# Kernel optimization log

Measured on AMD Instinct MI355X. Metric: run time of the kernel, lower is better.

Reference implementation:

```python
import jax, jax.numpy as jnp
import numpy as np

DIM = 192
HEADS = 6
HEAD_DIM = DIM // HEADS
WS = 8            # window size
N = WS * WS       # tokens per window
IN_CC = 16        # top-k kept keys per query
B, H, W = 8, 64, 64
NEG = -100.0      # value used by the torch code for masked logits
EPS_NORM = 1e-12  # F.normalize eps
EPS_LN = 1e-5     # nn.LayerNorm eps


def _rel_pos_index(ws):
    coords = np.stack(np.meshgrid(np.arange(ws), np.arange(ws), indexing='ij'))  # (2,ws,ws)
    cf = coords.reshape(2, -1)
    rel = (cf[:, :, None] - cf[:, None, :]).transpose(1, 2, 0).astype(np.int64)  # (N,N,2)
    rel[:, :, 0] += ws - 1
    rel[:, :, 1] += ws - 1
    rel[:, :, 0] *= 2 * ws - 1
    return jnp.asarray(rel.sum(-1))  # (N,N) indices into (2ws-1)^2 table

REL_IDX = _rel_pos_index(WS)


def _layer_norm(x, g, b):
    mu = jnp.mean(x, -1, keepdims=True)
    var = jnp.mean(jnp.square(x - mu), -1, keepdims=True)
    return (x - mu) * jax.lax.rsqrt(var + EPS_LN) * g + b


def _l2n(x):
    n = jnp.sqrt(jnp.sum(jnp.square(x), -1, keepdims=True))
    return x / jnp.maximum(n, EPS_NORM)


def setup_inputs() -> dict:
    key = jax.random.key(0)
    ks = jax.random.split(key, 8)
    s = 0.02
    return {
        'x': jax.random.normal(ks[0], (B, DIM, H, W), jnp.float32),
        'norm1_g': jnp.ones((DIM,), jnp.float32),
        'norm1_b': jnp.zeros((DIM,), jnp.float32),
        'qkv_w': jax.random.normal(ks[1], (3 * DIM, DIM), jnp.float32) * s,
        'qkv_b': jnp.zeros((3 * DIM,), jnp.float32),
        'proj_w': jax.random.normal(ks[2], (DIM, DIM), jnp.float32) * s,
        'proj_b': jnp.zeros((DIM,), jnp.float32),
        'rpb_table': jax.random.normal(ks[3], ((2 * WS - 1) ** 2, HEADS), jnp.float32) * s,
        'temperature': jnp.ones((HEADS, 1, 1), jnp.float32),
        'norm2_g': jnp.ones((DIM,), jnp.float32),
        'norm2_b': jnp.zeros((DIM,), jnp.float32),
        'fc1_w': jax.random.normal(ks[4], (4 * DIM, DIM), jnp.float32) * s,
        'fc1_b': jnp.zeros((4 * DIM,), jnp.float32),
        'fc2_w': jax.random.normal(ks[5], (DIM, 4 * DIM), jnp.float32) * s,
        'fc2_b': jnp.zeros((DIM,), jnp.float32),
    }


def reference(x, norm1_g, norm1_b, qkv_w, qkv_b, proj_w, proj_b, rpb_table,
              temperature, norm2_g, norm2_b, fc1_w, fc1_b, fc2_w, fc2_b):
    b, c, h, w = x.shape
    # (B,C,H,W) -> (B,L,C), pre-norm (note: the torch code norms the shortcut too)
    xs = jnp.transpose(x.reshape(b, c, h * w), (0, 2, 1))
    shortcut = _layer_norm(xs, norm1_g, norm1_b)  # (B,L,C)

    # window partition: (B,H,W,C) -> (B*nWh*nWw, N, C); shift_size=0, no padding (H,W % WS == 0)
    xin = shortcut.reshape(b, h // WS, WS, w // WS, WS, c)
    xin = jnp.transpose(xin, (0, 1, 3, 2, 4, 5)).reshape(-1, N, c)
    B_ = xin.shape[0]

    qkv = (xin @ qkv_w.T + qkv_b).reshape(B_, N, 3, HEADS, HEAD_DIM)
    qkv = jnp.transpose(qkv, (2, 0, 3, 1, 4))  # (3, B_, h, N, d)
    q, k, v = qkv[0], qkv[1], qkv[2]

    # cosine attention with learned per-head temperature
    attn = jnp.einsum('bhnd,bhmd->bhnm', _l2n(q), _l2n(k)) * temperature  # (B_,h,N,N)

    # top-k sparsification: keep IN_CC largest logits per query (threshold == kth value;
    # equivalent to the torch topk+scatter mask for distinct values)
    kth = jax.lax.top_k(attn, IN_CC)[0][..., -1:]
    attn = jnp.where(attn >= kth, attn, NEG)

    # relative position bias gather: (N,N,h) -> (h,N,N)
    rpb = jnp.transpose(rpb_table[REL_IDX], (2, 0, 1))
    attn = jax.nn.softmax(attn + rpb[None], axis=-1)

    out = jnp.einsum('bhnm,bhmd->bhnd', attn, v)
    out = jnp.transpose(out, (0, 2, 1, 3)).reshape(B_, N, c)
    out = out @ proj_w.T + proj_b

    # window reverse -> (B, L, C)
    out = out.reshape(b, h // WS, w // WS, WS, WS, c)
    out = jnp.transpose(out, (0, 1, 3, 2, 4, 5)).reshape(b, h * w, c)

    x2 = shortcut + out  # drop_path = identity (eval)
    hdn = _layer_norm(x2, norm2_g, norm2_b)
    hdn = jax.nn.gelu(hdn @ fc1_w.T + fc1_b, approximate=False) @ fc2_w.T + fc2_b
    x2 = x2 + hdn

    # back to (B,C,H,W)
    return jnp.transpose(x2, (0, 2, 1)).reshape(b, c, h, w)
```

## Files before the change

### kernel.cpp

```cpp
#include <hip/hip_runtime.h>
#include <hip/hip_bf16.h>
#include <math.h>

#define DIM     192
#define HEADS   6
#define HEAD_DIM 32
#define NTOK    64
#define IN_CC   16
#define TTOT    32768
#define NWIN    512

using bf16x8 = __attribute__((ext_vector_type(8))) short;
using f32x4  = __attribute__((ext_vector_type(4))) float;
typedef unsigned short ushort_t;

__device__ __forceinline__ ushort_t f2b(float f) {
    unsigned u = __float_as_uint(f);
    u += 0x7fffu + ((u >> 16) & 1u);
    return (ushort_t)(u >> 16);
}
__device__ __forceinline__ unsigned pk2(float a, float b) {
    return (unsigned)f2b(a) | ((unsigned)f2b(b) << 16);
}

__global__ __launch_bounds__(256) void cvt_all_kernel(
    const float* __restrict__ s0, const float* __restrict__ s1,
    const float* __restrict__ s2, const float* __restrict__ s3,
    ushort_t* __restrict__ d0, ushort_t* __restrict__ d1,
    ushort_t* __restrict__ d2, ushort_t* __restrict__ d3)
{
    const int bid = blockIdx.x;
    const float* src; ushort_t* dst; int off, K;
    if (bid < 108)      { src = s0; dst = d0; off = bid;       K = 192; }
    else if (bid < 144) { src = s1; dst = d1; off = bid - 108; K = 192; }
    else if (bid < 288) { src = s2; dst = d2; off = bid - 144; K = 192; }
    else                { src = s3; dst = d3; off = bid - 288; K = 768; }
    const int K8 = K >> 3;
    const int d  = (off * 256 + threadIdx.x) * 4;
    const int frag = d >> 7, win = d & 127;
    const int m16w = win >> 3, k7 = win & 7;
    const int oblk = frag / K8, kblk = frag - oblk * K8;
    const int o = oblk * 16 + m16w, k = kblk * 8 + k7;
    float4 v = *(const float4*)(src + (size_t)o * K + k);
    ushort4 ov;
    ov.x = f2b(v.x); ov.y = f2b(v.y); ov.z = f2b(v.z); ov.w = f2b(v.w);
    *(ushort4*)(dst + d) = ov;
}

__global__ __launch_bounds__(256) void ln1_kernel(
    const float* __restrict__ x, const float* __restrict__ g,
    const float* __restrict__ bb, float* __restrict__ outp,
    ushort_t* __restrict__ outh)
{
    __shared__ float xs[64][193];
    __shared__ float mu_s[64], rs_s[64];
    __shared__ float gs[192], bs[192];
    const int tid = threadIdx.x;
    const int t0  = blockIdx.x * 64;
    const int b   = t0 >> 12;
    const int hw0 = t0 & 4095;
    if (tid < 192) { gs[tid] = g[tid]; bs[tid] = bb[tid]; }
    const int tok = tid & 63, qq = tid >> 6;
    const float* xb = x + (size_t)b * (DIM * 4096) + hw0 + tok;
    #pragma unroll
    for (int it = 0; it < 48; ++it) {
        int c = it * 4 + qq;
        xs[tok][c] = xb[(size_t)c * 4096];
    }
    __syncthreads();
    const int tok2 = tid >> 2, p = tid & 3;
    float sum = 0.f;
    #pragma unroll
    for (int c = 0; c < 48; ++c) sum += xs[tok2][p * 48 + c];
    sum += __shfl_xor(sum, 1);
    sum += __shfl_xor(sum, 2);
    const float m = sum * (1.0f / 192.0f);
    float ss = 0.f;
    #pragma unroll
    for (int c = 0; c < 48; ++c) { float d = xs[tok2][p * 48 + c] - m; ss += d * d; }
    ss += __shfl_xor(ss, 1);
    ss += __shfl_xor(ss, 2);
    if (p == 0) {
        mu_s[tok2] = m;
        rs_s[tok2] = 1.0f / sqrtf(ss * (1.0f / 192.0f) + 1e-5f);
    }
    __syncthreads();
    float* ob = outp + (size_t)t0 * DIM;
    ushort_t* obh = outh + (size_t)t0 * DIM;
    #pragma unroll
    for (int it = 0; it < 48; ++it) {
        int idx = it * 256 + tid;
        int tk = idx / 192, c = idx % 192;
        float v = (xs[tk][c] - mu_s[tk]) * rs_s[tk] * gs[c] + bs[c];
        ob[idx] = v;
        obh[idx] = f2b(v);
    }
}

__global__ __launch_bounds__(256) void gemm_mfma(
    const ushort_t* __restrict__ A, const ushort_t* __restrict__ Wf,
    const float* __restrict__ bias, const float* __restrict__ res,
    float* __restrict__ outf, ushort_t* __restrict__ outh,
    int N, int K, int epi)
{
    __shared__ __align__(16) float Ct[4][32][68];
    const int tid  = threadIdx.x;
    const int wave = tid >> 6, lane = tid & 63;
    const int m16 = lane & 15, quad = lane >> 4;
    const int t0 = (blockIdx.x * 4 + wave) * 64, o0 = blockIdx.y * 64;
    const int K8 = K >> 3;
    float (*Cw)[68] = Ct[wave];

    f32x4 acc[4][4];
    #pragma unroll
    for (int i = 0; i < 4; ++i)
        #pragma unroll
        for (int j = 0; j < 4; ++j)
            acc[i][j] = (f32x4)(0.0f);

    const ushort_t* Ab = A + (size_t)t0 * K + quad * 8;
    const ushort_t* Wb = Wf + (size_t)(o0 >> 4) * K8 * 128 + m16 * 8;
    for (int ks = 0; ks < K; ks += 32) {
        bf16x8 af[4], wv[4];
        #pragma unroll
        for (int i = 0; i < 4; ++i)
            af[i] = *(const bf16x8*)(Ab + (size_t)(16 * i + m16) * K + ks);
        #pragma unroll
        for (int j = 0; j < 4; ++j)
            wv[j] = *(const bf16x8*)(Wb + (size_t)(j * K8 + (ks >> 3) + quad) * 128);
        #pragma unroll
        for (int i = 0; i < 4; ++i)
            #pragma unroll
            for (int j = 0; j < 4; ++j)
                acc[i][j] = __builtin_amdgcn_mfma_f32_16x16x32_bf16(wv[j], af[i], acc[i][j], 0, 0, 0);
    }

    float4 bj[4];
    #pragma unroll
    for (int j = 0; j < 4; ++j)
        bj[j] = *(const float4*)&bias[o0 + 16 * j + quad * 4];

    #pragma unroll
    for (int p = 0; p < 2; ++p) {
        #pragma unroll
        for (int ih = 0; ih < 2; ++ih) {
            const int i = 2 * p + ih;
            #pragma unroll
            for (int j = 0; j < 4; ++j) {
                f32x4 v = acc[i][j];
                v[0] += bj[j].x; v[1] += bj[j].y; v[2] += bj[j].z; v[3] += bj[j].w;
                *(f32x4*)&Cw[ih * 16 + m16][16 * j + quad * 4] = v;
            }
        }
        if (epi == 3) {
            #pragma unroll
            for (int q = 0; q < 4; ++q) {
                const int idx = q * 64 + lane;
                const int row = idx >> 3, c8 = (idx & 7) * 8;
                float4 f0 = *(const float4*)&Cw[row][c8];
                float4 f1 = *(const float4*)&Cw[row][c8 + 4];
                uint4 w;
                w.x = pk2(f0.x, f0.y); w.y = pk2(f0.z, f0.w);
                w.z = pk2(f1.x, f1.y); w.w = pk2(f1.z, f1.w);
                *(uint4*)&outh[(size_t)(t0 + p * 32 + row) * N + o0 + c8] = w;
            }
        } else {
            #pragma unroll
            for (int q = 0; q < 8; ++q) {
                const int idx = q * 64 + lane;
                const int row = idx >> 4, c4 = (idx & 15) * 4;
                float4 vv = *(const float4*)&Cw[row][c4];
                const size_t gidx = (size_t)(t0 + p * 32 + row) * N + o0 + c4;
                if (epi == 1) {
                    const float4 rv = *(const float4*)&res[gidx];
                    vv.x += rv.x; vv.y += rv.y; vv.z += rv.z; vv.w += rv.w;
                }
                *(float4*)&outf[gidx] = vv;
            }
        }
    }
}

__global__ __launch_bounds__(256) void mlp_fused(
    const float* __restrict__ x2, const ushort_t* __restrict__ w1f,
    const ushort_t* __restrict__ w2f, const float* __restrict__ fc1_b,
    const float* __restrict__ fc2_b, const float* __restrict__ g2,
    const float* __restrict__ b2, float* __restrict__ outp)
{
    __shared__ __align__(16) char smem[43008];
    ushort_t (*h_h)[200] = (ushort_t(*)[200])smem;
    ushort_t (*a1c)[136] = (ushort_t(*)[136])(smem + 25600);
    float* gs  = (float*)(smem + 25600);
    float* bs  = gs + 192;

    const int tid  = threadIdx.x;
    const int wave = tid >> 6, lane = tid & 63;
    const int m16 = lane & 15, quad = lane >> 4;
    const int t0 = blockIdx.x * 64;
    const int b   = t0 >> 12;
    const int hw0 = t0 & 4095;

    if (tid < 192) { gs[tid] = g2[tid]; bs[tid] = b2[tid]; }
    __syncthreads();
    {
        const int tok = tid >> 2, p = tid & 3;
        const float* rp = x2 + (size_t)(t0 + tok) * DIM + p * 48;
        float xv[48];
        #pragma unroll
        for (int c4 = 0; c4 < 12; ++c4)
            *(float4*)&xv[c4 * 4] = *(const float4*)(rp + c4 * 4);
        float sum = 0.f;
        #pragma unroll
        for (int c = 0; c < 48; ++c) sum += xv[c];
        sum += __shfl_xor(sum, 1);
        sum += __shfl_xor(sum, 2);
        const float m = sum * (1.0f / 192.0f);
        float ss = 0.f;
        #pragma unroll
        for (int c = 0; c < 48; ++c) { float d = xv[c] - m; ss += d * d; }
        ss += __shfl_xor(ss, 1);
        ss += __shfl_xor(ss, 2);
        const float rs = 1.0f / sqrtf(ss * (1.0f / 192.0f) + 1e-5f);
        ushort_t* hp = &h_h[tok][p * 48];
        #pragma unroll
        for (int c2 = 0; c2 < 24; ++c2) {
            float v0 = (xv[2*c2]   - m) * rs * gs[p * 48 + 2*c2]   + bs[p * 48 + 2*c2];
            float v1 = (xv[2*c2+1] - m) * rs * gs[p * 48 + 2*c2+1] + bs[p * 48 + 2*c2+1];
            *(unsigned*)(hp + 2 * c2) = pk2(v0, v1);
        }
    }
    __syncthreads();

    f32x4 acc2[4][3];
    #pragma unroll
    for (int i = 0; i < 4; ++i)
        #pragma unroll
        for (int j = 0; j < 3; ++j)
            acc2[i][j] = (f32x4)(0.0f);

    for (int c = 0; c < 6; ++c) {
        f32x4 acc1[4][2];
        #pragma unroll
        for (int i = 0; i < 4; ++i)
            #pragma unroll
            for (int j = 0; j < 2; ++j)
                acc1[i][j] = (f32x4)(0.0f);
        const ushort_t* Wb1 = w1f + (size_t)(c * 8 + wave * 2) * 24 * 128 + m16 * 8;
        for (int ks = 0; ks < 192; ks += 32) {
            bf16x8 af[4], wv[2];
            #pragma unroll
            for (int i = 0; i < 4; ++i)
                af[i] = *(const bf16x8*)&h_h[16 * i + m16][quad * 8 + ks];
            #pragma unroll
            for (int j = 0; j < 2; ++j)
                wv[j] = *(const bf16x8*)(Wb1 + (size_t)(j * 24 + (ks >> 3) + quad) * 128);
            #pragma unroll
            for (int i = 0; i < 4; ++i)
                #pragma unroll
                for (int j = 0; j < 2; ++j)
                    acc1[i][j] = __builtin_amdgcn_mfma_f32_16x16x32_bf16(wv[j], af[i], acc1[i][j], 0, 0, 0);
        }
        float2 b1j[2];
        #pragma unroll
        for (int j = 0; j < 2; ++j) {
            const int o = c * 128 + wave * 32 + 16 * j + quad * 4;
            b1j[j] = make_float2(0.f, 0.f);
        }
        #pragma unroll
        for (int j = 0; j < 2; ++j) {
            const int o = c * 128 + wave * 32 + 16 * j + quad * 4;
            const float4 bv = *(const float4*)&fc1_b[o];
            #pragma unroll
            for (int i = 0; i < 4; ++i) {
                f32x4 v = acc1[i][j];
                v[0] += bv.x; v[1] += bv.y; v[2] += bv.z; v[3] += bv.w;
                #pragma unroll
                for (int r = 0; r < 4; ++r) {
                    float xg = v[r];
                    float e1 = __expf(xg * (1.5957691f + 0.0713548f * xg * xg)) + 1.0f;
                    v[r] = xg - xg * __builtin_amdgcn_rcpf(e1);
                }
                uint2 pkd;
                pkd.x = pk2(v[0], v[1]); pkd.y = pk2(v[2], v[3]);
                *(uint2*)&a1c[16 * i + m16][wave * 32 + 16 * j + quad * 4] = pkd;
            }
        }
        __syncthreads();
        const ushort_t* Wb2 = w2f + (size_t)(wave * 3) * 96 * 128 + m16 * 8;
        for (int ks = 0; ks < 128; ks += 32) {
            bf16x8 af2[4], wv2[3];
            #pragma unroll
            for (int i = 0; i < 4; ++i)
                af2[i] = *(const bf16x8*)&a1c[16 * i + m16][quad * 8 + ks];
            #pragma unroll
            for (int j = 0; j < 3; ++j)
                wv2[j] = *(const bf16x8*)(Wb2 + (size_t)(j * 96 + c * 16 + (ks >> 3) + quad) * 128);
            #pragma unroll
            for (int i = 0; i < 4; ++i)
                #pragma unroll
                for (int j = 0; j < 3; ++j)
                    acc2[i][j] = __builtin_amdgcn_mfma_f32_16x16x32_bf16(wv2[j], af2[i], acc2[i][j], 0, 0, 0);
        }
        __syncthreads();
    }

    float (*Cw)[68] = (float(*)[68])(smem + wave * 8704);
    float4 b2j[3];
    #pragma unroll
    for (int j = 0; j < 3; ++j)
        b2j[j] = *(const float4*)&fc2_b[wave * 48 + 16 * j + quad * 4];
    #pragma unroll
    for (int p = 0; p < 2; ++p) {
        #pragma unroll
        for (int ih = 0; ih < 2; ++ih) {
            const int i = 2 * p + ih;
            #pragma unroll
            for (int j = 0; j < 3; ++j) {
                f32x4 v = acc2[i][j];
                v[0] += b2j[j].x; v[1] += b2j[j].y; v[2] += b2j[j].z; v[3] += b2j[j].w;
                *(f32x4*)&Cw[ih * 16 + m16][16 * j + quad * 4] = v;
            }
        }
        #pragma unroll
        for (int q = 0; q < 6; ++q) {
            const int idx = q * 64 + lane;
            const int cc = idx >> 3, t4 = (idx & 7) * 4;
            const int o  = wave * 48 + cc;
            const int tb = t0 + p * 32 + t4;
            float4 vv;
            vv.x = Cw[t4 + 0][cc] + x2[(size_t)(tb + 0) * DIM + o];
            vv.y = Cw[t4 + 1][cc] + x2[(size_t)(tb + 1) * DIM + o];
            vv.z = Cw[t4 + 2][cc] + x2[(size_t)(tb + 2) * DIM + o];
            vv.w = Cw[t4 + 3][cc] + x2[(size_t)(tb + 3) * DIM + o];
            *(float4*)&outp[(size_t)b * (DIM * 4096) + (size_t)o * 4096
                            + hw0 + p * 32 + t4] = vv;
        }
    }
}

__global__ __launch_bounds__(64) void attn_mfma_kernel(
    const ushort_t* __restrict__ qkvh, const float* __restrict__ rpb_table,
    const float* __restrict__ temp, ushort_t* __restrict__ outb)
{
    __shared__ __align__(16) char smem[16016];
    ushort_t* Qh  = (ushort_t*)smem;
    ushort_t* Kh  = (ushort_t*)(smem + 5120);
    float*    Ss  = (float*)smem;
    ushort_t* Pl  = (ushort_t*)smem;
    ushort_t* Vt  = (ushort_t*)(smem + 10240);
    float*    ksb = (float*)(smem + 14848);
    float*    rpb = (float*)(smem + 15104);

    const int n   = threadIdx.x;
    const int win = blockIdx.x;
    const int h   = blockIdx.y;
    const int b   = win >> 6;
    const int wh  = (win >> 3) & 7, ww = win & 7;
    const int i1  = n >> 3, j1 = n & 7;
    const int t   = b * 4096 + (wh * 8 + i1) * 64 + (ww * 8 + j1);
    const ushort_t* base = qkvh + (size_t)t * 576 + h * 32;
    const int m16 = n & 15, quad = n >> 4;

    unsigned qu[16], ku[16], vu[16];
    #pragma unroll
    for (int c = 0; c < 4; ++c) {
        ((uint4*)qu)[c] = *(const uint4*)(base + 8 * c);
        ((uint4*)ku)[c] = *(const uint4*)(base + 192 + 8 * c);
        ((uint4*)vu)[c] = *(const uint4*)(base + 384 + 8 * c);
    }
    float sq = 0.f, sk = 0.f;
    #pragma unroll
    for (int c = 0; c < 16; ++c) {
        float a0 = __uint_as_float(qu[c] << 16);
        float a1 = __uint_as_float(qu[c] & 0xffff0000u);
        sq += a0 * a0 + a1 * a1;
        float b0 = __uint_as_float(ku[c] << 16);
        float b1 = __uint_as_float(ku[c] & 0xffff0000u);
        sk += b0 * b0 + b1 * b1;
    }
    const float qs  = temp[h] / fmaxf(sqrtf(sq), 1e-12f);
    const float ksc = 1.0f / fmaxf(sqrtf(sk), 1e-12f);

    #pragma unroll
    for (int c = 0; c < 4; ++c) {
        *(uint4*)&Qh[n * 40 + 8 * c] = ((uint4*)qu)[c];
        *(uint4*)&Kh[n * 40 + 8 * c] = ((uint4*)ku)[c];
    }
    const int vslot = 4 * m16 + quad;
    #pragma unroll
    for (int d = 0; d < 16; ++d) {
        Vt[(2 * d) * 72 + vslot]     = (ushort_t)(vu[d] & 0xffffu);
        Vt[(2 * d + 1) * 72 + vslot] = (ushort_t)(vu[d] >> 16);
    }
    ksb[vslot] = ksc;
    for (int r = n; r < 225; r += 64) rpb[r] = rpb_table[r * 6 + h];
    __syncthreads();

    bf16x8 aq[4], bk[4];
    #pragma unroll
    for (int i = 0; i < 4; ++i) aq[i] = *(const bf16x8*)&Qh[(16*i + m16) * 40 + quad * 8];
    #pragma unroll
    for (int j = 0; j < 4; ++j) bk[j] = *(const bf16x8*)&Kh[(16*j + m16) * 40 + quad * 8];
    f32x4 acc[4][4];
    #pragma unroll
    for (int i = 0; i < 4; ++i)
        #pragma unroll
        for (int j = 0; j < 4; ++j)
            acc[i][j] = __builtin_amdgcn_mfma_f32_16x16x32_bf16(aq[i], bk[j], (f32x4)(0.0f), 0, 0, 0);
    __syncthreads();

    float s[64];
    #pragma unroll
    for (int i = 0; i < 2; ++i)
        #pragma unroll
        for (int r = 0; r < 4; ++r) {
            f32x4 vv = { acc[i][0][r], acc[i][1][r], acc[i][2][r], acc[i][3][r] };
            *(f32x4*)&Ss[(16 * i + 4 * quad + r) * 68 + 4 * m16] = vv;
        }
    __syncthreads();
    if (n < 32) {
        #pragma unroll
        for (int c = 0; c < 16; ++c)
            *(float4*)&s[4 * c] = *(const float4*)&Ss[n * 68 + 4 * c];
    }
    __syncthreads();
    #pragma unroll
    for (int i = 2; i < 4; ++i)
        #pragma unroll
        for (int r = 0; r < 4; ++r) {
            f32x4 vv = { acc[i][0][r], acc[i][1][r], acc[i][2][r], acc[i][3][r] };
            *(f32x4*)&Ss[(16 * (i - 2) + 4 * quad + r) * 68 + 4 * m16] = vv;
        }
    __syncthreads();
    if (n >= 32) {
        #pragma unroll
        for (int c = 0; c < 16; ++c)
            *(float4*)&s[4 * c] = *(const float4*)&Ss[(n - 32) * 68 + 4 * c];
    }

    #pragma unroll
    for (int c = 0; c < 16; ++c) {
        float4 kv = *(const float4*)&ksb[4 * c];
        s[4*c+0] *= qs * kv.x; s[4*c+1] *= qs * kv.y;
        s[4*c+2] *= qs * kv.z; s[4*c+3] *= qs * kv.w;
    }

    float thr = 1e30f;
    for (int it = 0; it < IN_CC; ++it) {
        float mx = -1e30f;
        #pragma unroll
        for (int m = 0; m < 64; ++m) {
            float vv = (s[m] < thr) ? s[m] : -1e30f;
            mx = fmaxf(mx, vv);
        }
        thr = mx;
    }

    const int basen = i1 * 15 + j1;
    float mx = -1e30f;
    #pragma unroll
    for (int c = 0; c < 64; ++c) {
        const int m = 16 * (c & 3) + (c >> 2);
        const int i2 = m >> 3, j2 = m & 7;
        float vv = ((s[c] >= thr) ? s[c] : -100.0f)
                 + rpb[basen + (7 - i2) * 15 + (7 - j2)];
        s[c] = vv;
        mx = fmaxf(mx, vv);
    }
    float sum = 0.f;
    #pragma unroll
    for (int c = 0; c < 64; ++c) { float e = __expf(s[c] - mx); s[c] = e; sum += e; }
    const float inv = 1.0f / sum;
    #pragma unroll
    for (int c = 0; c < 64; ++c) s[c] *= inv;

    __syncthreads();
    #pragma unroll
    for (int gix = 0; gix < 8; ++gix) {
        uint4 w;
        w.x = pk2(s[8*gix+0], s[8*gix+1]); w.y = pk2(s[8*gix+2], s[8*gix+3]);
        w.z = pk2(s[8*gix+4], s[8*gix+5]); w.w = pk2(s[8*gix+6], s[8*gix+7]);
        *(uint4*)&Pl[n * 72 + 8 * gix] = w;
    }
    __syncthreads();

    f32x4 o[4][2];
    #pragma unroll
    for (int i = 0; i < 4; ++i)
        #pragma unroll
        for (int j2 = 0; j2 < 2; ++j2)
            o[i][j2] = (f32x4)(0.0f);
    #pragma unroll
    for (int kh = 0; kh < 64; kh += 32) {
        bf16x8 pa[4], vb[2];
        #pragma unroll
        for (int i = 0; i < 4; ++i)
            pa[i] = *(const bf16x8*)&Pl[(16*i + m16) * 72 + kh + quad * 8];
        #pragma unroll
        for (int j2 = 0; j2 < 2; ++j2)
            vb[j2] = *(const bf16x8*)&Vt[(16*j2 + m16) * 72 + kh + quad * 8];
        #pragma unroll
        for (int i = 0; i < 4; ++i)
            #pragma unroll
            for (int j2 = 0; j2 < 2; ++j2)
                o[i][j2] = __builtin_amdgcn_mfma_f32_16x16x32_bf16(pa[i], vb[j2], o[i][j2], 0, 0, 0);
    }

    #pragma unroll
    for (int i = 0; i < 4; ++i) {
        #pragma unroll
        for (int r = 0; r < 4; ++r) {
            const int row = 16 * i + 4 * quad + r;
            const int tt  = b * 4096 + (wh * 8 + (row >> 3)) * 64 + ww * 8 + (row & 7);
            ushort_t* op = outb + (size_t)tt * DIM + h * 32;
            op[m16]      = f2b(o[i][0][r]);
            op[m16 + 16] = f2b(o[i][1][r]);
        }
    }
}

extern "C" void kernel_launch(void* const* d_in, const int* in_sizes, int n_in,
                              void* d_out, int out_size, void* d_ws, size_t ws_size,
                              hipStream_t stream)
{
    const float* x        = (const float*)d_in[0];
    const float* norm1_g  = (const float*)d_in[1];
    const float* norm1_b  = (const float*)d_in[2];
    const float* qkv_w    = (const float*)d_in[3];
    const float* qkv_b    = (const float*)d_in[4];
    const float* proj_w   = (const float*)d_in[5];
    const float* proj_b   = (const float*)d_in[6];
    const float* rpbt     = (const float*)d_in[7];
    const float* temp     = (const float*)d_in[8];
    const float* norm2_g  = (const float*)d_in[9];
    const float* norm2_b  = (const float*)d_in[10];
    const float* fc1_w    = (const float*)d_in[11];
    const float* fc1_b    = (const float*)d_in[12];
    const float* fc2_w    = (const float*)d_in[13];
    const float* fc2_b    = (const float*)d_in[14];
    float* out = (float*)d_out;

    char* wsb = (char*)d_ws;
    float*    shortcut   = (float*)wsb;
    ushort_t* shortcut_h = (ushort_t*)(wsb + 25165824);
    ushort_t* qkvh       = (ushort_t*)(wsb + 37748736);
    float*    x2         = (float*)(wsb + 88080384);
    ushort_t* attnout_h  = (ushort_t*)(wsb + 113246208);
    ushort_t* wq  = (ushort_t*)(wsb + 125829120);
    ushort_t* wp  = wq + 110592;
    ushort_t* w1  = wp + 36864;
    ushort_t* w2  = w1 + 147456;

    hipLaunchKernelGGL(cvt_all_kernel, dim3(432), dim3(256), 0, stream,
                       qkv_w, proj_w, fc1_w, fc2_w, wq, wp, w1, w2);

    hipLaunchKernelGGL(ln1_kernel, dim3(TTOT / 64), dim3(256), 0, stream,
                       x, norm1_g, norm1_b, shortcut, shortcut_h);
    hipLaunchKernelGGL(gemm_mfma, dim3(TTOT / 256, 9), dim3(256), 0, stream,
                       shortcut_h, wq, qkv_b, (const float*)nullptr,
                       (float*)nullptr, qkvh, 576, 192, 3);
    hipLaunchKernelGGL(attn_mfma_kernel, dim3(NWIN, HEADS), dim3(64), 0, stream,
                       qkvh, rpbt, temp, attnout_h);
    hipLaunchKernelGGL(gemm_mfma, dim3(TTOT / 256, 3), dim3(256), 0, stream,
                       attnout_h, wp, proj_b, shortcut,
                       x2, (ushort_t*)nullptr, 192, 192, 1);
    hipLaunchKernelGGL(mlp_fused, dim3(TTOT / 64), dim3(256), 0, stream,
                       x2, w1, w2, fc1_b, fc2_b, norm2_g, norm2_b, out);
}
```

Baseline: 217.8 us.

## Fuse window attention with output projection and residual add

Replaces the per-(window,head) attention kernel and the separate projection GEMM with one kernel per window that uses six waves, one per head. The head outputs are gathered into a shared-memory tile and projected with MFMA, then proj bias and the shortcut are added and x2 is written directly. This removes the bf16 attention-output round trip through global memory and one launch. In exchange each block uses about 96 KB of LDS, which lowers occupancy, and the intra-wave __syncthreads now synchronise all six waves. It also drops an unused bias temp in the MLP.

```diff
diff --git a/kernel.cpp b/kernel.cpp
--- a/kernel.cpp
+++ b/kernel.cpp
@@ -181,6 +181,240 @@
     }
 }
 
+__global__ __launch_bounds__(384) void attn_proj_fused(
+    const ushort_t* __restrict__ qkvh, const float* __restrict__ rpb_table,
+    const float* __restrict__ temp, const ushort_t* __restrict__ wpf,
+    const float* __restrict__ proj_b, const float* __restrict__ shortcut,
+    float* __restrict__ x2)
+{
+    __shared__ __align__(16) char smem[96768];
+    const int tid  = threadIdx.x;
+    const int wave = tid >> 6, n = tid & 63;
+    char* arena = smem + wave * 16128;
+    ushort_t* Qh  = (ushort_t*)arena;
+    ushort_t* Kh  = (ushort_t*)(arena + 5120);
+    float*    Ss  = (float*)arena;
+    ushort_t* Pl  = (ushort_t*)arena;
+    ushort_t* Vt  = (ushort_t*)(arena + 10240);
+    float*    ksb = (float*)(arena + 14848);
+    float*    rpb = (float*)(arena + 15104);
+    ushort_t (*AoT)[200] = (ushort_t(*)[200])smem;
+    float* Cww = (float*)(smem + 25600 + wave * 9216);
+
+    const int win = blockIdx.x;
+    const int h   = wave;
+    const int b   = win >> 6;
+    const int wh  = (win >> 3) & 7, ww = win & 7;
+    const int i1  = n >> 3, j1 = n & 7;
+    const int t   = b * 4096 + (wh * 8 + i1) * 64 + (ww * 8 + j1);
+    const ushort_t* base = qkvh + (size_t)t * 576 + h * 32;
+    const int m16 = n & 15, quad = n >> 4;
+
+    unsigned qu[16], ku[16], vu[16];
+    #pragma unroll
+    for (int c = 0; c < 4; ++c) {
+        ((uint4*)qu)[c] = *(const uint4*)(base + 8 * c);
+        ((uint4*)ku)[c] = *(const uint4*)(base + 192 + 8 * c);
+        ((uint4*)vu)[c] = *(const uint4*)(base + 384 + 8 * c);
+    }
+    float sq = 0.f, sk = 0.f;
+    #pragma unroll
+    for (int c = 0; c < 16; ++c) {
+        float a0 = __uint_as_float(qu[c] << 16);
+        float a1 = __uint_as_float(qu[c] & 0xffff0000u);
+        sq += a0 * a0 + a1 * a1;
+        float b0 = __uint_as_float(ku[c] << 16);
+        float b1 = __uint_as_float(ku[c] & 0xffff0000u);
+        sk += b0 * b0 + b1 * b1;
+    }
+    const float qs  = temp[h] / fmaxf(sqrtf(sq), 1e-12f);
+    const float ksc = 1.0f / fmaxf(sqrtf(sk), 1e-12f);
+
+    #pragma unroll
+    for (int c = 0; c < 4; ++c) {
+        *(uint4*)&Qh[n * 40 + 8 * c] = ((uint4*)qu)[c];
+        *(uint4*)&Kh[n * 40 + 8 * c] = ((uint4*)ku)[c];
+    }
+    const int vslot = 4 * m16 + quad;
+    #pragma unroll
+    for (int d = 0; d < 16; ++d) {
+        Vt[(2 * d) * 72 + vslot]     = (ushort_t)(vu[d] & 0xffffu);
+        Vt[(2 * d + 1) * 72 + vslot] = (ushort_t)(vu[d] >> 16);
+    }
+    ksb[vslot] = ksc;
+    for (int r = n; r < 225; r += 64) rpb[r] = rpb_table[r * 6 + h];
+    __syncthreads();
+
+    bf16x8 aq[4], bk[4];
+    #pragma unroll
+    for (int i = 0; i < 4; ++i) aq[i] = *(const bf16x8*)&Qh[(16*i + m16) * 40 + quad * 8];
+    #pragma unroll
+    for (int j = 0; j < 4; ++j) bk[j] = *(const bf16x8*)&Kh[(16*j + m16) * 40 + quad * 8];
+    f32x4 acc[4][4];
+    #pragma unroll
+    for (int i = 0; i < 4; ++i)
+        #pragma unroll
+        for (int j = 0; j < 4; ++j)
+            acc[i][j] = __builtin_amdgcn_mfma_f32_16x16x32_bf16(aq[i], bk[j], (f32x4)(0.0f), 0, 0, 0);
+    __syncthreads();
+
+    float s[64];
+    #pragma unroll
+    for (int i = 0; i < 2; ++i)
+        #pragma unroll
+        for (int r = 0; r < 4; ++r) {
+            f32x4 vv = { acc[i][0][r], acc[i][1][r], acc[i][2][r], acc[i][3][r] };
+            *(f32x4*)&Ss[(16 * i + 4 * quad + r) * 68 + 4 * m16] = vv;
+        }
+    __syncthreads();
+    if (n < 32) {
+        #pragma unroll
+        for (int c = 0; c < 16; ++c)
+            *(float4*)&s[4 * c] = *(const float4*)&Ss[n * 68 + 4 * c];
+    }
+    __syncthreads();
+    #pragma unroll
+    for (int i = 2; i < 4; ++i)
+        #pragma unroll
+        for (int r = 0; r < 4; ++r) {
+            f32x4 vv = { acc[i][0][r], acc[i][1][r], acc[i][2][r], acc[i][3][r] };
+            *(f32x4*)&Ss[(16 * (i - 2) + 4 * quad + r) * 68 + 4 * m16] = vv;
+        }
+    __syncthreads();
+    if (n >= 32) {
+        #pragma unroll
+        for (int c = 0; c < 16; ++c)
+            *(float4*)&s[4 * c] = *(const float4*)&Ss[(n - 32) * 68 + 4 * c];
+    }
+
+    #pragma unroll
+    for (int c = 0; c < 16; ++c) {
+        float4 kv = *(const float4*)&ksb[4 * c];
+        s[4*c+0] *= qs * kv.x; s[4*c+1] *= qs * kv.y;
+        s[4*c+2] *= qs * kv.z; s[4*c+3] *= qs * kv.w;
+    }
+
+    float thr = 1e30f;
+    for (int it = 0; it < IN_CC; ++it) {
+        float mx = -1e30f;
+        #pragma unroll
+        for (int m = 0; m < 64; ++m) {
+            float vv = (s[m] < thr) ? s[m] : -1e30f;
+            mx = fmaxf(mx, vv);
+        }
+        thr = mx;
+    }
+
+    const int basen = i1 * 15 + j1;
+    float mx = -1e30f;
+    #pragma unroll
+    for (int c = 0; c < 64; ++c) {
+        const int m = 16 * (c & 3) + (c >> 2);
+        const int i2 = m >> 3, j2 = m & 7;
+        float vv = ((s[c] >= thr) ? s[c] : -100.0f)
+                 + rpb[basen + (7 - i2) * 15 + (7 - j2)];
+        s[c] = vv;
+        mx = fmaxf(mx, vv);
+    }
+    float sum = 0.f;
+    #pragma unroll
+    for (int c = 0; c < 64; ++c) { float e = __expf(s[c] - mx); s[c] = e; sum += e; }
+    const float inv = 1.0f / sum;
+    #pragma unroll
+    for (int c = 0; c < 64; ++c) s[c] *= inv;
+
+    __syncthreads();
+    #pragma unroll
+    for (int gix = 0; gix < 8; ++gix) {
+        uint4 w;
+        w.x = pk2(s[8*gix+0], s[8*gix+1]); w.y = pk2(s[8*gix+2], s[8*gix+3]);
+        w.z = pk2(s[8*gix+4], s[8*gix+5]); w.w = pk2(s[8*gix+6], s[8*gix+7]);
+        *(uint4*)&Pl[n * 72 + 8 * gix] = w;
+    }
+    __syncthreads();
+
+    f32x4 o[4][2];
+    #pragma unroll
+    for (int i = 0; i < 4; ++i)
+        #pragma unroll
+        for (int j2 = 0; j2 < 2; ++j2)
+            o[i][j2] = (f32x4)(0.0f);
+    #pragma unroll
+    for (int kh = 0; kh < 64; kh += 32) {
+        bf16x8 pa[4], vb[2];
+        #pragma unroll
+        for (int i = 0; i < 4; ++i)
+            pa[i] = *(const bf16x8*)&Pl[(16*i + m16) * 72 + kh + quad * 8];
+        #pragma unroll
+        for (int j2 = 0; j2 < 2; ++j2)
+            vb[j2] = *(const bf16x8*)&Vt[(16*j2 + m16) * 72 + kh + quad * 8];
+        #pragma unroll
+        for (int i = 0; i < 4; ++i)
+            #pragma unroll
+            for (int j2 = 0; j2 < 2; ++j2)
+                o[i][j2] = __builtin_amdgcn_mfma_f32_16x16x32_bf16(pa[i], vb[j2], o[i][j2], 0, 0, 0);
+    }
+    __syncthreads();
+
+    #pragma unroll
+    for (int i = 0; i < 4; ++i) {
+        #pragma unroll
+        for (int r = 0; r < 4; ++r) {
+            const int row = 16 * i + 4 * quad + r;
+            AoT[row][h * 32 + m16]      = f2b(o[i][0][r]);
+            AoT[row][h * 32 + 16 + m16] = f2b(o[i][1][r]);
+        }
+    }
+    __syncthreads();
+
+    f32x4 pacc[4][2];
+    #pragma unroll
+    for (int i = 0; i < 4; ++i)
+        #pragma unroll
+        for (int j = 0; j < 2; ++j)
+            pacc[i][j] = (f32x4)(0.0f);
+    const ushort_t* Wb = wpf + (size_t)(wave * 2) * 24 * 128 + m16 * 8;
+    for (int ks = 0; ks < 192; ks += 32) {
+        bf16x8 af[4], wv[2];
+        #pragma unroll
+        for (int i = 0; i < 4; ++i)
+            af[i] = *(const bf16x8*)&AoT[16 * i + m16][quad * 8 + ks];
+        #pragma unroll
+        for (int j = 0; j < 2; ++j)
+            wv[j] = *(const bf16x8*)(Wb + (size_t)(j * 24 + (ks >> 3) + quad) * 128);
+        #pragma unroll
+        for (int i = 0; i < 4; ++i)
+            #pragma unroll
+            for (int j = 0; j < 2; ++j)
+                pacc[i][j] = __builtin_amdgcn_mfma_f32_16x16x32_bf16(wv[j], af[i], pacc[i][j], 0, 0, 0);
+    }
+
+    float4 bj[2];
+    #pragma unroll
+    for (int j = 0; j < 2; ++j)
+        bj[j] = *(const float4*)&proj_b[wave * 32 + 16 * j + quad * 4];
+    #pragma unroll
+    for (int i = 0; i < 4; ++i)
+        #pragma unroll
+        for (int j = 0; j < 2; ++j) {
+            f32x4 v = pacc[i][j];
+            v[0] += bj[j].x; v[1] += bj[j].y; v[2] += bj[j].z; v[3] += bj[j].w;
+            *(f32x4*)&Cww[(16 * i + m16) * 36 + 16 * j + quad * 4] = v;
+        }
+
+    #pragma unroll
+    for (int q = 0; q < 8; ++q) {
+        const int idx = q * 64 + n;
+        const int row = idx >> 3, c4 = (idx & 7) * 4;
+        const int ii = row >> 3, jj = row & 7;
+        const int tt = b * 4096 + (wh * 8 + ii) * 64 + ww * 8 + jj;
+        float4 vv = *(const float4*)&Cww[row * 36 + c4];
+        const float4 rv = *(const float4*)&shortcut[(size_t)tt * DIM + wave * 32 + c4];
+        vv.x += rv.x; vv.y += rv.y; vv.z += rv.z; vv.w += rv.w;
+        *(float4*)&x2[(size_t)tt * DIM + wave * 32 + c4] = vv;
+    }
+}
+
 __global__ __launch_bounds__(256) void mlp_fused(
     const float* __restrict__ x2, const ushort_t* __restrict__ w1f,
     const ushort_t* __restrict__ w2f, const float* __restrict__ fc1_b,
@@ -259,12 +493,6 @@
                 #pragma unroll
                 for (int j = 0; j < 2; ++j)
                     acc1[i][j] = __builtin_amdgcn_mfma_f32_16x16x32_bf16(wv[j], af[i], acc1[i][j], 0, 0, 0);
-        }
-        float2 b1j[2];
-        #pragma unroll
-        for (int j = 0; j < 2; ++j) {
-            const int o = c * 128 + wave * 32 + 16 * j + quad * 4;
-            b1j[j] = make_float2(0.f, 0.f);
         }
         #pragma unroll
         for (int j = 0; j < 2; ++j) {
@@ -334,187 +562,6 @@
             vv.w = Cw[t4 + 3][cc] + x2[(size_t)(tb + 3) * DIM + o];
             *(float4*)&outp[(size_t)b * (DIM * 4096) + (size_t)o * 4096
                             + hw0 + p * 32 + t4] = vv;
-        }
-    }
-}
-
-__global__ __launch_bounds__(64) void attn_mfma_kernel(
-    const ushort_t* __restrict__ qkvh, const float* __restrict__ rpb_table,
-    const float* __restrict__ temp, ushort_t* __restrict__ outb)
-{
-    __shared__ __align__(16) char smem[16016];
-    ushort_t* Qh  = (ushort_t*)smem;
-    ushort_t* Kh  = (ushort_t*)(smem + 5120);
-    float*    Ss  = (float*)smem;
-    ushort_t* Pl  = (ushort_t*)smem;
-    ushort_t* Vt  = (ushort_t*)(smem + 10240);
-    float*    ksb = (float*)(smem + 14848);
-    float*    rpb = (float*)(smem + 15104);
-
-    const int n   = threadIdx.x;
-    const int win = blockIdx.x;
-    const int h   = blockIdx.y;
-    const int b   = win >> 6;
-    const int wh  = (win >> 3) & 7, ww = win & 7;
-    const int i1  = n >> 3, j1 = n & 7;
-    const int t   = b * 4096 + (wh * 8 + i1) * 64 + (ww * 8 + j1);
-    const ushort_t* base = qkvh + (size_t)t * 576 + h * 32;
-    const int m16 = n & 15, quad = n >> 4;
-
-    unsigned qu[16], ku[16], vu[16];
-    #pragma unroll
-    for (int c = 0; c < 4; ++c) {
-        ((uint4*)qu)[c] = *(const uint4*)(base + 8 * c);
-        ((uint4*)ku)[c] = *(const uint4*)(base + 192 + 8 * c);
-        ((uint4*)vu)[c] = *(const uint4*)(base + 384 + 8 * c);
-    }
-    float sq = 0.f, sk = 0.f;
-    #pragma unroll
-    for (int c = 0; c < 16; ++c) {
-        float a0 = __uint_as_float(qu[c] << 16);
-        float a1 = __uint_as_float(qu[c] & 0xffff0000u);
-        sq += a0 * a0 + a1 * a1;
-        float b0 = __uint_as_float(ku[c] << 16);
-        float b1 = __uint_as_float(ku[c] & 0xffff0000u);
-        sk += b0 * b0 + b1 * b1;
-    }
-    const float qs  = temp[h] / fmaxf(sqrtf(sq), 1e-12f);
-    const float ksc = 1.0f / fmaxf(sqrtf(sk), 1e-12f);
-
-    #pragma unroll
-    for (int c = 0; c < 4; ++c) {
-        *(uint4*)&Qh[n * 40 + 8 * c] = ((uint4*)qu)[c];
-        *(uint4*)&Kh[n * 40 + 8 * c] = ((uint4*)ku)[c];
-    }
-    const int vslot = 4 * m16 + quad;
-    #pragma unroll
-    for (int d = 0; d < 16; ++d) {
-        Vt[(2 * d) * 72 + vslot]     = (ushort_t)(vu[d] & 0xffffu);
-        Vt[(2 * d + 1) * 72 + vslot] = (ushort_t)(vu[d] >> 16);
-    }
-    ksb[vslot] = ksc;
-    for (int r = n; r < 225; r += 64) rpb[r] = rpb_table[r * 6 + h];
-    __syncthreads();
-
-    bf16x8 aq[4], bk[4];
-    #pragma unroll
-    for (int i = 0; i < 4; ++i) aq[i] = *(const bf16x8*)&Qh[(16*i + m16) * 40 + quad * 8];
-    #pragma unroll
-    for (int j = 0; j < 4; ++j) bk[j] = *(const bf16x8*)&Kh[(16*j + m16) * 40 + quad * 8];
-    f32x4 acc[4][4];
-    #pragma unroll
-    for (int i = 0; i < 4; ++i)
-        #pragma unroll
-        for (int j = 0; j < 4; ++j)
-            acc[i][j] = __builtin_amdgcn_mfma_f32_16x16x32_bf16(aq[i], bk[j], (f32x4)(0.0f), 0, 0, 0);
-    __syncthreads();
-
-    float s[64];
-    #pragma unroll
-    for (int i = 0; i < 2; ++i)
-        #pragma unroll
-        for (int r = 0; r < 4; ++r) {
-            f32x4 vv = { acc[i][0][r], acc[i][1][r], acc[i][2][r], acc[i][3][r] };
-            *(f32x4*)&Ss[(16 * i + 4 * quad + r) * 68 + 4 * m16] = vv;
-        }
-    __syncthreads();
-    if (n < 32) {
-        #pragma unroll
-        for (int c = 0; c < 16; ++c)
-            *(float4*)&s[4 * c] = *(const float4*)&Ss[n * 68 + 4 * c];
-    }
-    __syncthreads();
-    #pragma unroll
-    for (int i = 2; i < 4; ++i)
-        #pragma unroll
-        for (int r = 0; r < 4; ++r) {
-            f32x4 vv = { acc[i][0][r], acc[i][1][r], acc[i][2][r], acc[i][3][r] };
-            *(f32x4*)&Ss[(16 * (i - 2) + 4 * quad + r) * 68 + 4 * m16] = vv;
-        }
-    __syncthreads();
-    if (n >= 32) {
-        #pragma unroll
-        for (int c = 0; c < 16; ++c)
-            *(float4*)&s[4 * c] = *(const float4*)&Ss[(n - 32) * 68 + 4 * c];
-    }
-
-    #pragma unroll
-    for (int c = 0; c < 16; ++c) {
-        float4 kv = *(const float4*)&ksb[4 * c];
-        s[4*c+0] *= qs * kv.x; s[4*c+1] *= qs * kv.y;
-        s[4*c+2] *= qs * kv.z; s[4*c+3] *= qs * kv.w;
-    }
-
-    float thr = 1e30f;
-    for (int it = 0; it < IN_CC; ++it) {
-        float mx = -1e30f;
-        #pragma unroll
-        for (int m = 0; m < 64; ++m) {
-            float vv = (s[m] < thr) ? s[m] : -1e30f;
-            mx = fmaxf(mx, vv);
-        }
-        thr = mx;
-    }
-
-    const int basen = i1 * 15 + j1;
-    float mx = -1e30f;
-    #pragma unroll
-    for (int c = 0; c < 64; ++c) {
-        const int m = 16 * (c & 3) + (c >> 2);
-        const int i2 = m >> 3, j2 = m & 7;
-        float vv = ((s[c] >= thr) ? s[c] : -100.0f)
-                 + rpb[basen + (7 - i2) * 15 + (7 - j2)];
-        s[c] = vv;
-        mx = fmaxf(mx, vv);
-    }
-    float sum = 0.f;
-    #pragma unroll
-    for (int c = 0; c < 64; ++c) { float e = __expf(s[c] - mx); s[c] = e; sum += e; }
-    const float inv = 1.0f / sum;
-    #pragma unroll
-    for (int c = 0; c < 64; ++c) s[c] *= inv;
-
-    __syncthreads();
-    #pragma unroll
-    for (int gix = 0; gix < 8; ++gix) {
-        uint4 w;
-        w.x = pk2(s[8*gix+0], s[8*gix+1]); w.y = pk2(s[8*gix+2], s[8*gix+3]);
-        w.z = pk2(s[8*gix+4], s[8*gix+5]); w.w = pk2(s[8*gix+6], s[8*gix+7]);
-        *(uint4*)&Pl[n * 72 + 8 * gix] = w;
-    }
-    __syncthreads();
-
-    f32x4 o[4][2];
-    #pragma unroll
-    for (int i = 0; i < 4; ++i)
-        #pragma unroll
-        for (int j2 = 0; j2 < 2; ++j2)
-            o[i][j2] = (f32x4)(0.0f);
-    #pragma unroll
-    for (int kh = 0; kh < 64; kh += 32) {
-        bf16x8 pa[4], vb[2];
-        #pragma unroll
-        for (int i = 0; i < 4; ++i)
-            pa[i] = *(const bf16x8*)&Pl[(16*i + m16) * 72 + kh + quad * 8];
-        #pragma unroll
-        for (int j2 = 0; j2 < 2; ++j2)
-            vb[j2] = *(const bf16x8*)&Vt[(16*j2 + m16) * 72 + kh + quad * 8];
-        #pragma unroll
-        for (int i = 0; i < 4; ++i)
-            #pragma unroll
-            for (int j2 = 0; j2 < 2; ++j2)
-                o[i][j2] = __builtin_amdgcn_mfma_f32_16x16x32_bf16(pa[i], vb[j2], o[i][j2], 0, 0, 0);
-    }
-
-    #pragma unroll
-    for (int i = 0; i < 4; ++i) {
-        #pragma unroll
-        for (int r = 0; r < 4; ++r) {
-            const int row = 16 * i + 4 * quad + r;
-            const int tt  = b * 4096 + (wh * 8 + (row >> 3)) * 64 + ww * 8 + (row & 7);
-            ushort_t* op = outb + (size_t)tt * DIM + h * 32;
-            op[m16]      = f2b(o[i][0][r]);
-            op[m16 + 16] = f2b(o[i][1][r]);
         }
     }
 }
@@ -545,7 +592,6 @@
     ushort_t* shortcut_h = (ushort_t*)(wsb + 25165824);
     ushort_t* qkvh       = (ushort_t*)(wsb + 37748736);
     float*    x2         = (float*)(wsb + 88080384);
-    ushort_t* attnout_h  = (ushort_t*)(wsb + 113246208);
     ushort_t* wq  = (ushort_t*)(wsb + 125829120);
     ushort_t* wp  = wq + 110592;
     ushort_t* w1  = wp + 36864;
@@ -559,11 +605,8 @@
     hipLaunchKernelGGL(gemm_mfma, dim3(TTOT / 256, 9), dim3(256), 0, stream,
                        shortcut_h, wq, qkv_b, (const float*)nullptr,
                        (float*)nullptr, qkvh, 576, 192, 3);
-    hipLaunchKernelGGL(attn_mfma_kernel, dim3(NWIN, HEADS), dim3(64), 0, stream,
-                       qkvh, rpbt, temp, attnout_h);
-    hipLaunchKernelGGL(gemm_mfma, dim3(TTOT / 256, 3), dim3(256), 0, stream,
-                       attnout_h, wp, proj_b, shortcut,
-                       x2, (ushort_t*)nullptr, 192, 192, 1);
+    hipLaunchKernelGGL(attn_proj_fused, dim3(NWIN), dim3(384), 0, stream,
+                       qkvh, rpbt, temp, wp, proj_b, shortcut, x2);
     hipLaunchKernelGGL(mlp_fused, dim3(TTOT / 64), dim3(256), 0, stream,
                        x2, w1, w2, fc1_b, fc2_b, norm2_g, norm2_b, out);
 }
```

Measured after the change: 217.3 us. No clear change (-0.2%).
